# Kernel tuning notes

Measured on AMD Instinct MI355X. Metric: run time of the kernel, lower is better.

Reference implementation:

```python
import jax, jax.numpy as jnp
import numpy as np

B, N, D, H, NB = 64, 2048, 256, 64, 3
TOPK_RATIO = 0.1
LN_EPS = 1e-5
NEG_INF = -1e30


def setup_inputs() -> dict:
    key = jax.random.key(0)
    ks = jax.random.split(key, 16)
    s = 0.02
    return {
        "instances": jax.random.normal(ks[0], (B, N, D), dtype=jnp.float32),
        "mask": jnp.ones((B, N), dtype=jnp.float32),
        # top-k scorer: Linear(D,64) -> ReLU -> Linear(64,1)
        "Ws1": jax.random.normal(ks[1], (D, H), dtype=jnp.float32) * s,
        "bs1": jnp.zeros((H,), dtype=jnp.float32),
        "Ws2": jax.random.normal(ks[2], (H,), dtype=jnp.float32) * s,
        "bs2": jnp.zeros((), dtype=jnp.float32),
        # NB attention branches stacked: Linear(D,64) -> Tanh -> Linear(64,1)
        "Wa1": jax.random.normal(ks[3], (NB, D, H), dtype=jnp.float32) * s,
        "ba1": jnp.zeros((NB, H), dtype=jnp.float32),
        "Wa2": jax.random.normal(ks[4], (NB, H), dtype=jnp.float32) * s,
        "ba2": jnp.zeros((NB,), dtype=jnp.float32),
        # fusion: Linear(5D, 2D) -> LayerNorm -> GELU -> Linear(2D, 2D)
        "Wf1": jax.random.normal(ks[5], ((2 + NB) * D, 2 * D), dtype=jnp.float32) * s,
        "bf1": jnp.zeros((2 * D,), dtype=jnp.float32),
        "ln_g": jnp.ones((2 * D,), dtype=jnp.float32),
        "ln_b": jnp.zeros((2 * D,), dtype=jnp.float32),
        "Wf2": jax.random.normal(ks[6], (2 * D, 2 * D), dtype=jnp.float32) * s,
        "bf2": jnp.zeros((2 * D,), dtype=jnp.float32),
    }


def _forward(instances, mask, Ws1, bs1, Ws2, bs2, Wa1, ba1, Wa2, ba2,
             Wf1, bf1, ln_g, ln_b, Wf2, bf2):
    invalid = mask == 0  # [B, N]

    # ---- mean pooling (masked) ----
    valid_counts = jnp.sum(mask, axis=1, keepdims=True)  # [B,1]
    mean_pooled = jnp.einsum("bnd,bn->bd", instances, mask) / jnp.maximum(valid_counts, 1.0)

    # ---- top-k pooling ----
    h = jax.nn.relu(jnp.einsum("bnd,dh->bnh", instances, Ws1) + bs1)
    tk_scores = jnp.einsum("bnh,h->bn", h, Ws2) + bs2  # [B, N]
    tk_scores = jnp.where(invalid, NEG_INF, tk_scores)
    # torch code computes per-sample k but only uses max_k; with all-ones mask
    # max_k == int(N * ratio) (static) -- replicated faithfully.
    max_k = max(1, int(N * TOPK_RATIO))
    _, topk_idx = jax.lax.top_k(tk_scores, max_k)  # [B, max_k]
    topk_mask = jnp.zeros((B, N), dtype=instances.dtype)
    topk_mask = topk_mask.at[jnp.arange(B)[:, None], topk_idx].set(1.0)
    combined = topk_mask * mask
    denom = jnp.maximum(jnp.sum(combined, axis=1, keepdims=True), 1.0)
    topk_pooled = jnp.einsum("bnd,bn->bd", instances, combined) / denom

    # ---- multi-branch attention (vectorized over branches) ----
    ah = jnp.tanh(jnp.einsum("bnd,kdh->kbnh", instances, Wa1) + ba1[:, None, None, :])
    a_scores = jnp.einsum("kbnh,kh->kbn", ah, Wa2) + ba2[:, None, None]  # [NB,B,N]
    a_scores = jnp.where(invalid[None], NEG_INF, a_scores)
    attn = jax.nn.softmax(a_scores, axis=-1)
    attn = jnp.where(invalid[None], 0.0, attn)  # [NB, B, N]
    branch_pooled = jnp.einsum("kbn,bnd->kbd", attn, instances)  # [NB, B, D]

    # ---- fusion MLP ----
    cat = jnp.concatenate(
        [mean_pooled, topk_pooled, branch_pooled.transpose(1, 0, 2).reshape(B, NB * D)],
        axis=-1,
    )  # [B, (2+NB)*D]
    x = cat @ Wf1 + bf1
    mu = jnp.mean(x, axis=-1, keepdims=True)
    var = jnp.mean(jnp.square(x - mu), axis=-1, keepdims=True)
    x = (x - mu) * jax.lax.rsqrt(var + LN_EPS) * ln_g + ln_b
    x = jax.nn.gelu(x, approximate=False)  # torch nn.GELU default = exact erf
    bag_embedding = x @ Wf2 + bf2  # [B, 2D]

    # ---- attention diagnostics ----
    all_attn = attn.transpose(1, 0, 2)  # [B, NB, N]
    avg_attn = jnp.mean(all_attn, axis=1)  # [B, N]
    entropy = -jnp.sum(avg_attn * jnp.log(avg_attn + 1e-8), axis=-1)
    effective_n = 1.0 / jnp.sum(jnp.square(avg_attn), axis=-1)
    k5 = max(1, int(N * 0.05))
    top5_mass = jnp.sum(jax.lax.top_k(avg_attn, k5)[0], axis=-1)
    return bag_embedding, all_attn, avg_attn, topk_mask, entropy, effective_n, top5_mass


def reference(instances, mask, Ws1, bs1, Ws2, bs2, Wa1, ba1, Wa2, ba2,
              Wf1, bf1, ln_g, ln_b, Wf2, bf2):
    return _forward(instances, mask, Ws1, bs1, Ws2, bs2, Wa1, ba1, Wa2, ba2,
                    Wf1, bf1, ln_g, ln_b, Wf2, bf2)
```

## Files before the change

kernel.cpp:

```cpp
#include <hip/hip_runtime.h>
#include <stdint.h>

constexpr int B_ = 64, N_ = 2048, D_ = 256, H_ = 64;
constexpr int M_ = B_ * N_;
constexpr int TOPK_ = 204, TOP5_ = 102;
constexpr float NEGINF_ = -1e30f;

constexpr int OUT_BAG  = 0;
constexpr int OUT_ATTN = 32768;
constexpr int OUT_AVG  = OUT_ATTN + 393216;
constexpr int OUT_TOPK = OUT_AVG + 131072;
constexpr int OUT_ENT  = OUT_TOPK + 131072;
constexpr int OUT_EFF  = OUT_ENT + 64;
constexpr int OUT_T5   = OUT_EFF + 64;

constexpr int WS_TK    = 0;
constexpr int WS_SC    = 131072;
constexpr int WS_STATS = WS_SC + 393216;
constexpr int WS_PART  = WS_STATS + 128;
constexpr int WS_BFRAG = WS_PART + 655360;
constexpr int WS_X1    = WS_BFRAG + 32768;
constexpr int WS_G     = WS_X1 + 32768;

typedef short  bf16x8 __attribute__((ext_vector_type(8)));
typedef float  f32x4  __attribute__((ext_vector_type(4)));

__device__ __forceinline__ short cvt_bf16(float f) {
    unsigned u = __float_as_uint(f);
    unsigned r = (u + 0x7FFFu + ((u >> 16) & 1u)) >> 16;
    return (short)r;
}
__device__ __forceinline__ unsigned pack_bf16x2(float a, float b) {
    return (unsigned)(unsigned short)cvt_bf16(a) | ((unsigned)(unsigned short)cvt_bf16(b) << 16);
}
__device__ __forceinline__ float tanh_fast(float x) {
    float e = __expf(2.0f * x);
    return 1.0f - 2.0f / (e + 1.0f);
}
__device__ __forceinline__ unsigned flip_f32(float f) {
    unsigned u = __float_as_uint(f);
    return (u & 0x80000000u) ? ~u : (u | 0x80000000u);
}
__device__ __forceinline__ float unflip_f32(unsigned u) {
    unsigned b = (u & 0x80000000u) ? (u & 0x7FFFFFFFu) : ~u;
    return __uint_as_float(b);
}

__device__ __forceinline__ float block_sum256(float v, volatile float* red, int t) {
    #pragma unroll
    for (int off = 32; off; off >>= 1) v += __shfl_xor(v, off, 64);
    __syncthreads();
    if ((t & 63) == 0) red[t >> 6] = v;
    __syncthreads();
    return red[0] + red[1] + red[2] + red[3];
}
__device__ __forceinline__ float block_max256(float v, volatile float* red, int t) {
    #pragma unroll
    for (int off = 32; off; off >>= 1) v = fmaxf(v, __shfl_xor(v, off, 64));
    __syncthreads();
    if ((t & 63) == 0) red[t >> 6] = v;
    __syncthreads();
    return fmaxf(fmaxf(red[0], red[1]), fmaxf(red[2], red[3]));
}

__device__ unsigned radix_kth(const unsigned* key, int n, int k,
                              unsigned* hist, int* sdig, int t, int* rem_out)
{
    unsigned prefix = 0;
    int kk = k;
    #pragma unroll
    for (int pass = 0; pass < 4; ++pass) {
        const int shift = 24 - 8 * pass;
        const unsigned hi_mask = (pass == 0) ? 0u : (0xFFFFFFFFu << (shift + 8));
        hist[t] = 0;
        __syncthreads();
        for (int i = t; i < n; i += 256) {
            unsigned u = key[i];
            if ((u & hi_mask) == (prefix & hi_mask))
                atomicAdd(&hist[(u >> shift) & 0xFFu], 1u);
        }
        __syncthreads();
        for (int s = 1; s < 256; s <<= 1) {
            unsigned v = (t + s < 256) ? hist[t + s] : 0u;
            __syncthreads();
            hist[t] += v;
            __syncthreads();
        }
        if (t == 0) *sdig = 0;
        __syncthreads();
        if ((int)hist[t] >= kk) atomicMax(sdig, t);
        __syncthreads();
        const int dig = *sdig;
        if (dig < 255) kk -= (int)hist[dig + 1];
        prefix |= (unsigned)dig << shift;
        __syncthreads();
    }
    *rem_out = kk;
    return prefix;
}

__global__ __launch_bounds__(256)
void k_prep(const float* __restrict__ Ws1, const float* __restrict__ Wa1,
            short* __restrict__ wsB)
{
    const int id = blockIdx.x * 256 + threadIdx.x;
    if (id >= 16384) return;
    const int lane = id & 63, ct = (id >> 6) & 15, c = id >> 10;
    const int col = ct * 16 + (lane & 15);
    const int kb  = c * 32 + ((lane >> 4) << 3);
    bf16x8 v;
    #pragma unroll
    for (int j = 0; j < 8; ++j) {
        const int k = kb + j;
        float w = (col < 64) ? Ws1[(size_t)k * H_ + col]
                             : Wa1[(((size_t)(col >> 6) - 1) * D_ + k) * H_ + (col & 63)];
        v[j] = cvt_bf16(w);
    }
    *(bf16x8*)(wsB + (size_t)id * 8) = v;
}

__global__ __launch_bounds__(256)
void k_scores(const float* __restrict__ inst, const float* __restrict__ mask,
              const short* __restrict__ wsB,
              const float* __restrict__ bs1, const float* __restrict__ Ws2,
              const float* __restrict__ bs2,
              const float* __restrict__ ba1, const float* __restrict__ Wa2,
              const float* __restrict__ ba2,
              float* __restrict__ ws)
{
    __shared__ unsigned xas[8192];
    const int t = threadIdx.x;
    const int s = t >> 6, l = t & 63;
    const int li = l & 15, qu = l >> 4;
    const int row0 = blockIdx.x * 64;

    {
        const float4* src = (const float4*)(inst + (size_t)row0 * D_);
        #pragma unroll
        for (int i = 0; i < 16; ++i) {
            const int f = i * 256 + t;
            const int row = f >> 6, k4 = f & 63;
            float4 x = src[f];
            const int base = ((k4 >> 3) * 256) + ((row >> 4) * 64) + (((k4 >> 1) & 3) * 16) + (row & 15);
            const int ui = base * 4 + (k4 & 1) * 2;
            xas[ui]     = pack_bf16x2(x.x, x.y);
            xas[ui + 1] = pack_bf16x2(x.z, x.w);
        }
    }
    __syncthreads();

    f32x4 acc[4][4];
    #pragma unroll
    for (int rt = 0; rt < 4; ++rt)
        #pragma unroll
        for (int c4 = 0; c4 < 4; ++c4) acc[rt][c4] = (f32x4){0.f, 0.f, 0.f, 0.f};

    const bf16x8* Bg = (const bf16x8*)wsB;
    bf16x8 bcur[4], bnxt[4];
    #pragma unroll
    for (int c4 = 0; c4 < 4; ++c4) bcur[c4] = Bg[(0 * 16 + s * 4 + c4) * 64 + l];

    #pragma unroll
    for (int c = 0; c < 8; ++c) {
        if (c < 7) {
            #pragma unroll
            for (int c4 = 0; c4 < 4; ++c4) bnxt[c4] = Bg[((c + 1) * 16 + s * 4 + c4) * 64 + l];
        }
        #pragma unroll
        for (int rt = 0; rt < 4; ++rt) {
            bf16x8 a = ((const bf16x8*)xas)[(c * 4 + rt) * 64 + l];
            #pragma unroll
            for (int c4 = 0; c4 < 4; ++c4)
                acc[rt][c4] = __builtin_amdgcn_mfma_f32_16x16x32_bf16(a, bcur[c4], acc[rt][c4], 0, 0, 0);
        }
        #pragma unroll
        for (int c4 = 0; c4 < 4; ++c4) bcur[c4] = bnxt[c4];
    }

    float bias[4], w2v[4];
    #pragma unroll
    for (int c4 = 0; c4 < 4; ++c4) {
        const int h = c4 * 16 + li;
        if (s == 0) { bias[c4] = bs1[h];                w2v[c4] = Ws2[h]; }
        else        { bias[c4] = ba1[(s - 1) * H_ + h]; w2v[c4] = Wa2[(s - 1) * H_ + h]; }
    }
    const float b2 = (s == 0) ? bs2[0] : ba2[s - 1];
    float* dst = (s == 0) ? (ws + WS_TK) : (ws + WS_SC + (size_t)(s - 1) * M_);

    #pragma unroll
    for (int rt = 0; rt < 4; ++rt) {
        #pragma unroll
        for (int i = 0; i < 4; ++i) {
            float p = 0.0f;
            #pragma unroll
            for (int c4 = 0; c4 < 4; ++c4) {
                float v = acc[rt][c4][i] + bias[c4];
                p += (s == 0 ? fmaxf(v, 0.0f) : tanh_fast(v)) * w2v[c4];
            }
            #pragma unroll
            for (int off = 1; off < 16; off <<= 1) p += __shfl_xor(p, off, 64);
            if (li == 0) {
                const int gr = row0 + rt * 16 + qu * 4 + i;
                dst[gr] = (mask[gr] == 0.0f) ? NEGINF_ : (p + b2);
            }
        }
    }
}

__global__ __launch_bounds__(256)
void k_batch(const float* __restrict__ ws_tk, const float* __restrict__ ws_sc,
             const float* __restrict__ mask,
             float* __restrict__ out_topk, float* __restrict__ ws_stats,
             float* __restrict__ out_attn, float* __restrict__ out_avg,
             float* __restrict__ out_ent, float* __restrict__ out_eff,
             float* __restrict__ out_t5)
{
    __shared__ float attn_s[3][N_];
    __shared__ unsigned ukey[N_];
    __shared__ unsigned hist[256];
    __shared__ int sdig, tie_cnt;
    __shared__ float red[4];
    const int b = blockIdx.x, t = threadIdx.x;

    float vsum = 0.0f;
    for (int i = t; i < N_; i += 256) {
        ukey[i] = flip_f32(ws_tk[b * N_ + i]);
        vsum += mask[b * N_ + i];
        out_topk[b * N_ + i] = 0.0f;
    }
    float vs = block_sum256(vsum, red, t);
    if (t == 0) { ws_stats[b] = vs; tie_cnt = 0; }
    __syncthreads();
    int rem;
    unsigned T = radix_kth(ukey, N_, TOPK_, hist, &sdig, t, &rem);
    float csum = 0.0f;
    for (int i = t; i < N_; i += 256) {
        const unsigned u = ukey[i];
        bool take = (u > T);
        if (!take && u == T) take = (atomicAdd(&tie_cnt, 1) < rem);
        if (take) {
            out_topk[b * N_ + i] = 1.0f;
            csum += mask[b * N_ + i];
        }
    }
    float cs = block_sum256(csum, red, t);
    if (t == 0) ws_stats[64 + b] = cs;

    for (int s = 0; s < 3; ++s) {
        const float* src = ws_sc + ((size_t)s * B_ + b) * N_;
        float fv[8];
        float mx = -3.4e38f;
        #pragma unroll
        for (int m = 0; m < 8; ++m) { fv[m] = src[t + 256 * m]; mx = fmaxf(mx, fv[m]); }
        float bm = block_max256(mx, red, t);
        float sm = 0.0f;
        #pragma unroll
        for (int m = 0; m < 8; ++m) { fv[m] = expf(fv[m] - bm); sm += fv[m]; }
        float tot = block_sum256(sm, red, t);
        float inv = 1.0f / tot;
        float* dst = out_attn + ((size_t)b * 3 + s) * N_;
        #pragma unroll
        for (int m = 0; m < 8; ++m) {
            float a = fv[m] * inv;
            attn_s[s][t + 256 * m] = a;
            dst[t + 256 * m] = a;
        }
    }
    __syncthreads();

    float esum = 0.0f, qsum = 0.0f;
    for (int i = t; i < N_; i += 256) {
        float a = (attn_s[0][i] + attn_s[1][i] + attn_s[2][i]) * (1.0f / 3.0f);
        out_avg[b * N_ + i] = a;
        esum -= a * logf(a + 1e-8f);
        qsum += a * a;
        ukey[i] = flip_f32(a);
    }
    float es = block_sum256(esum, red, t);
    float qs = block_sum256(qsum, red, t);
    if (t == 0) { out_ent[b] = es; out_eff[b] = 1.0f / qs; }
    __syncthreads();
    T = radix_kth(ukey, N_, TOP5_, hist, &sdig, t, &rem);
    float tsum = 0.0f;
    for (int i = t; i < N_; i += 256) {
        const unsigned u = ukey[i];
        if (u > T) tsum += unflip_f32(u);
    }
    float ts = block_sum256(tsum, red, t);
    if (t == 0) out_t5[b] = ts + (float)rem * unflip_f32(T);
}

__global__ __launch_bounds__(256)
void k_pool(const float* __restrict__ inst, const float* __restrict__ mask,
            const float* __restrict__ out_topk, const float* __restrict__ out_attn,
            float* __restrict__ ws_part)
{
    __shared__ float wgt[5][256];
    __shared__ float4 partial[4][5][64];
    const int blk = blockIdx.x;
    const int b = blk >> 3, ch = blk & 7;
    const int n0 = ch * 256;
    const int t = threadIdx.x;
    const int w = t >> 6, l = t & 63;
    {
        float mv = mask[b * N_ + n0 + t];
        wgt[0][t] = mv;
        wgt[1][t] = out_topk[b * N_ + n0 + t] * mv;
        const float* ab = out_attn + (size_t)b * 3 * N_ + n0 + t;
        wgt[2][t] = ab[0];
        wgt[3][t] = ab[N_];
        wgt[4][t] = ab[2 * N_];
    }
    __syncthreads();
    float4 a0 = {0,0,0,0}, a1 = {0,0,0,0}, a2 = {0,0,0,0}, a3 = {0,0,0,0}, a4 = {0,0,0,0};
    const float4* xp = (const float4*)(inst + ((size_t)b * N_ + n0 + w * 64) * D_) + l;
    #pragma unroll 4
    for (int nn = 0; nn < 64; ++nn) {
        float4 x = xp[(size_t)nn * 64];
        float w0 = wgt[0][w * 64 + nn], w1 = wgt[1][w * 64 + nn];
        float w2 = wgt[2][w * 64 + nn], w3 = wgt[3][w * 64 + nn];
        float w4 = wgt[4][w * 64 + nn];
        a0.x = fmaf(x.x, w0, a0.x); a0.y = fmaf(x.y, w0, a0.y);
        a0.z = fmaf(x.z, w0, a0.z); a0.w = fmaf(x.w, w0, a0.w);
        a1.x = fmaf(x.x, w1, a1.x); a1.y = fmaf(x.y, w1, a1.y);
        a1.z = fmaf(x.z, w1, a1.z); a1.w = fmaf(x.w, w1, a1.w);
        a2.x = fmaf(x.x, w2, a2.x); a2.y = fmaf(x.y, w2, a2.y);
        a2.z = fmaf(x.z, w2, a2.z); a2.w = fmaf(x.w, w2, a2.w);
        a3.x = fmaf(x.x, w3, a3.x); a3.y = fmaf(x.y, w3, a3.y);
        a3.z = fmaf(x.z, w3, a3.z); a3.w = fmaf(x.w, w3, a3.w);
        a4.x = fmaf(x.x, w4, a4.x); a4.y = fmaf(x.y, w4, a4.y);
        a4.z = fmaf(x.z, w4, a4.z); a4.w = fmaf(x.w, w4, a4.w);
    }
    partial[w][0][l] = a0; partial[w][1][l] = a1; partial[w][2][l] = a2;
    partial[w][3][l] = a3; partial[w][4][l] = a4;
    __syncthreads();
    for (int idx = t; idx < 320; idx += 256) {
        const int j = idx >> 6, l2 = idx & 63;
        float4 s0 = partial[0][j][l2], s1 = partial[1][j][l2];
        float4 s2 = partial[2][j][l2], s3 = partial[3][j][l2];
        float4 sm;
        sm.x = s0.x + s1.x + s2.x + s3.x;
        sm.y = s0.y + s1.y + s2.y + s3.y;
        sm.z = s0.z + s1.z + s2.z + s3.z;
        sm.w = s0.w + s1.w + s2.w + s3.w;
        *(float4*)(ws_part + (size_t)blk * 1280 + j * 256 + l2 * 4) = sm;
    }
}

__global__ __launch_bounds__(256)
void k_fuse1(const float* __restrict__ ws_part, const float* __restrict__ ws_stats,
             const float* __restrict__ Wf1, const float* __restrict__ bf1,
             float* __restrict__ x1)
{
    __shared__ float cl[1280];
    __shared__ float part[256];
    const int blk = blockIdx.x;
    const int b = blk >> 3, c = blk & 7;
    const int t = threadIdx.x;
    const float inv0 = 1.0f / fmaxf(ws_stats[b], 1.0f);
    const float inv1 = 1.0f / fmaxf(ws_stats[64 + b], 1.0f);
    for (int i = t; i < 1280; i += 256) {
        const int j = i >> 8, d = i & 255;
        float s = 0.0f;
        #pragma unroll
        for (int cc = 0; cc < 8; ++cc)
            s += ws_part[((size_t)(b * 8 + cc) * 5 + j) * 256 + d];
        if (j == 0)      s *= inv0;
        else if (j == 1) s *= inv1;
        cl[i] = s;
    }
    __syncthreads();
    const int j = c * 64 + (t & 63);
    const int s = t >> 6;
    float acc = 0.0f;
    const float* wp = Wf1 + (size_t)(s * 320) * 512 + j;
    #pragma unroll 8
    for (int i = 0; i < 320; ++i)
        acc = fmaf(cl[s * 320 + i], wp[(size_t)i * 512], acc);
    part[t] = acc;
    __syncthreads();
    if (t < 64)
        x1[b * 512 + c * 64 + t] =
            part[t] + part[64 + t] + part[128 + t] + part[192 + t] + bf1[c * 64 + t];
}

__global__ __launch_bounds__(256)
void k_fuse2(const float* __restrict__ x1, const float* __restrict__ ln_g,
             const float* __restrict__ ln_b, float* __restrict__ g)
{
    __shared__ float red[4];
    const int b = blockIdx.x, t = threadIdx.x;
    float v0 = x1[b * 512 + t], v1 = x1[b * 512 + 256 + t];
    float mu = block_sum256(v0 + v1, red, t) * (1.0f / 512.0f);
    float d0 = v0 - mu, d1 = v1 - mu;
    float var = block_sum256(d0 * d0 + d1 * d1, red, t) * (1.0f / 512.0f);
    float is = 1.0f / sqrtf(var + 1e-5f);
    float y0 = d0 * is * ln_g[t] + ln_b[t];
    float y1 = d1 * is * ln_g[t + 256] + ln_b[t + 256];
    g[b * 512 + t]       = 0.5f * y0 * (1.0f + erff(y0 * 0.70710678118654752440f));
    g[b * 512 + 256 + t] = 0.5f * y1 * (1.0f + erff(y1 * 0.70710678118654752440f));
}

__global__ __launch_bounds__(256)
void k_fuse3(const float* __restrict__ g, const float* __restrict__ Wf2,
             const float* __restrict__ bf2, float* __restrict__ out_bag)
{
    __shared__ float gl[512];
    __shared__ float part[256];
    const int blk = blockIdx.x;
    const int b = blk >> 3, c = blk & 7;
    const int t = threadIdx.x;
    const int j = c * 64 + (t & 63);
    const int s = t >> 6;
    for (int i = t; i < 512; i += 256) gl[i] = g[b * 512 + i];
    __syncthreads();
    float acc = 0.0f;
    const float* wp = Wf2 + (size_t)(s * 128) * 512 + j;
    #pragma unroll 8
    for (int i = 0; i < 128; ++i)
        acc = fmaf(gl[s * 128 + i], wp[(size_t)i * 512], acc);
    part[t] = acc;
    __syncthreads();
    if (t < 64)
        out_bag[b * 512 + c * 64 + t] =
            part[t] + part[64 + t] + part[128 + t] + part[192 + t] + bf2[c * 64 + t];
}

extern "C" void kernel_launch(void* const* d_in, const int* in_sizes, int n_in,
                              void* d_out, int out_size, void* d_ws, size_t ws_size,
                              hipStream_t stream)
{
    (void)in_sizes; (void)n_in; (void)out_size; (void)ws_size;
    const float* inst = (const float*)d_in[0];
    const float* mask = (const float*)d_in[1];
    const float* Ws1  = (const float*)d_in[2];
    const float* bs1  = (const float*)d_in[3];
    const float* Ws2  = (const float*)d_in[4];
    const float* bs2  = (const float*)d_in[5];
    const float* Wa1  = (const float*)d_in[6];
    const float* ba1  = (const float*)d_in[7];
    const float* Wa2  = (const float*)d_in[8];
    const float* ba2  = (const float*)d_in[9];
    const float* Wf1  = (const float*)d_in[10];
    const float* bf1  = (const float*)d_in[11];
    const float* lng  = (const float*)d_in[12];
    const float* lnb  = (const float*)d_in[13];
    const float* Wf2  = (const float*)d_in[14];
    const float* bf2  = (const float*)d_in[15];

    float* out = (float*)d_out;
    float* ws  = (float*)d_ws;
    short* wsB = (short*)(ws + WS_BFRAG);

    k_prep<<<64, 256, 0, stream>>>(Ws1, Wa1, wsB);
    k_scores<<<M_ / 64, 256, 0, stream>>>(inst, mask, wsB, bs1, Ws2, bs2,
                                          ba1, Wa2, ba2, ws);
    k_batch<<<B_, 256, 0, stream>>>(ws + WS_TK, ws + WS_SC, mask,
                                    out + OUT_TOPK, ws + WS_STATS,
                                    out + OUT_ATTN, out + OUT_AVG,
                                    out + OUT_ENT, out + OUT_EFF, out + OUT_T5);
    k_pool<<<B_ * 8, 256, 0, stream>>>(inst, mask, out + OUT_TOPK, out + OUT_ATTN,
                                       ws + WS_PART);
    k_fuse1<<<B_ * 8, 256, 0, stream>>>(ws + WS_PART, ws + WS_STATS, Wf1, bf1,
                                        ws + WS_X1);
    k_fuse2<<<B_, 256, 0, stream>>>(ws + WS_X1, lng, lnb, ws + WS_G);
    k_fuse3<<<B_ * 8, 256, 0, stream>>>(ws + WS_G, Wf2, bf2, out + OUT_BAG);
}
```

Measured before the change: 347.4 us.

## Keep weight fragments in registers and loop over four row tiles per block

k_scores now loads all 32 B-weight fragments into registers once per block and processes four 64-row tiles per block (512 blocks instead of 2048). This amortises the weight loads across tiles. The instance staging is changed to 32-byte row loads with an XOR-swizzled LDS layout to reduce bank conflicts. Launch bounds request 2 blocks per SM. The large register array (32 bf16x8) plus accumulators adds register pressure and may limit occupancy or cause spills, and the per-tile load is not overlapped with the MFMA work.

```diff
diff --git a/kernel.cpp b/kernel.cpp
--- a/kernel.cpp
+++ b/kernel.cpp
@@ -22,8 +22,9 @@
 constexpr int WS_X1    = WS_BFRAG + 32768;
 constexpr int WS_G     = WS_X1 + 32768;
 
-typedef short  bf16x8 __attribute__((ext_vector_type(8)));
-typedef float  f32x4  __attribute__((ext_vector_type(4)));
+typedef short    bf16x8 __attribute__((ext_vector_type(8)));
+typedef float    f32x4  __attribute__((ext_vector_type(4)));
+typedef unsigned u32x4  __attribute__((ext_vector_type(4)));
 
 __device__ __forceinline__ short cvt_bf16(float f) {
     unsigned u = __float_as_uint(f);
@@ -119,7 +120,7 @@
     *(bf16x8*)(wsB + (size_t)id * 8) = v;
 }
 
-__global__ __launch_bounds__(256)
+__global__ __launch_bounds__(256, 2)
 void k_scores(const float* __restrict__ inst, const float* __restrict__ mask,
               const short* __restrict__ wsB,
               const float* __restrict__ bs1, const float* __restrict__ Ws2,
@@ -132,49 +133,15 @@
     const int t = threadIdx.x;
     const int s = t >> 6, l = t & 63;
     const int li = l & 15, qu = l >> 4;
-    const int row0 = blockIdx.x * 64;
-
+
+    bf16x8 breg[32];
     {
-        const float4* src = (const float4*)(inst + (size_t)row0 * D_);
-        #pragma unroll
-        for (int i = 0; i < 16; ++i) {
-            const int f = i * 256 + t;
-            const int row = f >> 6, k4 = f & 63;
-            float4 x = src[f];
-            const int base = ((k4 >> 3) * 256) + ((row >> 4) * 64) + (((k4 >> 1) & 3) * 16) + (row & 15);
-            const int ui = base * 4 + (k4 & 1) * 2;
-            xas[ui]     = pack_bf16x2(x.x, x.y);
-            xas[ui + 1] = pack_bf16x2(x.z, x.w);
-        }
-    }
-    __syncthreads();
-
-    f32x4 acc[4][4];
-    #pragma unroll
-    for (int rt = 0; rt < 4; ++rt)
-        #pragma unroll
-        for (int c4 = 0; c4 < 4; ++c4) acc[rt][c4] = (f32x4){0.f, 0.f, 0.f, 0.f};
-
-    const bf16x8* Bg = (const bf16x8*)wsB;
-    bf16x8 bcur[4], bnxt[4];
-    #pragma unroll
-    for (int c4 = 0; c4 < 4; ++c4) bcur[c4] = Bg[(0 * 16 + s * 4 + c4) * 64 + l];
-
-    #pragma unroll
-    for (int c = 0; c < 8; ++c) {
-        if (c < 7) {
-            #pragma unroll
-            for (int c4 = 0; c4 < 4; ++c4) bnxt[c4] = Bg[((c + 1) * 16 + s * 4 + c4) * 64 + l];
-        }
-        #pragma unroll
-        for (int rt = 0; rt < 4; ++rt) {
-            bf16x8 a = ((const bf16x8*)xas)[(c * 4 + rt) * 64 + l];
+        const bf16x8* Bg = (const bf16x8*)wsB;
+        #pragma unroll
+        for (int c = 0; c < 8; ++c)
             #pragma unroll
             for (int c4 = 0; c4 < 4; ++c4)
-                acc[rt][c4] = __builtin_amdgcn_mfma_f32_16x16x32_bf16(a, bcur[c4], acc[rt][c4], 0, 0, 0);
-        }
-        #pragma unroll
-        for (int c4 = 0; c4 < 4; ++c4) bcur[c4] = bnxt[c4];
+                breg[c * 4 + c4] = Bg[(c * 16 + s * 4 + c4) * 64 + l];
     }
 
     float bias[4], w2v[4];
@@ -187,21 +154,67 @@
     const float b2 = (s == 0) ? bs2[0] : ba2[s - 1];
     float* dst = (s == 0) ? (ws + WS_TK) : (ws + WS_SC + (size_t)(s - 1) * M_);
 
-    #pragma unroll
-    for (int rt = 0; rt < 4; ++rt) {
-        #pragma unroll
-        for (int i = 0; i < 4; ++i) {
-            float p = 0.0f;
+    const int srow = t >> 5;
+    const int sk0  = 8 * (t & 31);
+    const int sc   = (t & 31) >> 2;
+    const int sq   = t & 3;
+
+    for (int tt = 0; tt < 4; ++tt) {
+        const int row0 = blockIdx.x * 256 + tt * 64;
+        __syncthreads();
+        {
+            const float* xb = inst + (size_t)row0 * D_ + sk0;
             #pragma unroll
-            for (int c4 = 0; c4 < 4; ++c4) {
-                float v = acc[rt][c4][i] + bias[c4];
-                p += (s == 0 ? fmaxf(v, 0.0f) : tanh_fast(v)) * w2v[c4];
+            for (int i = 0; i < 8; ++i) {
+                const float* rp = xb + (size_t)(i * 8 + srow) * D_;
+                float4 x = *(const float4*)rp;
+                float4 y = *(const float4*)(rp + 4);
+                const int lslot = (i & 1) * 8 + srow;
+                const int slot = (sc * 4 + (i >> 1)) * 64 + sq * 16 + (lslot ^ sc);
+                u32x4 v;
+                v[0] = pack_bf16x2(x.x, x.y);
+                v[1] = pack_bf16x2(x.z, x.w);
+                v[2] = pack_bf16x2(y.x, y.y);
+                v[3] = pack_bf16x2(y.z, y.w);
+                *(u32x4*)&xas[slot * 4] = v;
             }
+        }
+        __syncthreads();
+
+        f32x4 acc[4][4];
+        #pragma unroll
+        for (int rt = 0; rt < 4; ++rt)
             #pragma unroll
-            for (int off = 1; off < 16; off <<= 1) p += __shfl_xor(p, off, 64);
-            if (li == 0) {
-                const int gr = row0 + rt * 16 + qu * 4 + i;
-                dst[gr] = (mask[gr] == 0.0f) ? NEGINF_ : (p + b2);
+            for (int c4 = 0; c4 < 4; ++c4) acc[rt][c4] = (f32x4){0.f, 0.f, 0.f, 0.f};
+
+        #pragma unroll
+        for (int c = 0; c < 8; ++c) {
+            #pragma unroll
+            for (int rt = 0; rt < 4; ++rt) {
+                bf16x8 a = ((const bf16x8*)xas)[(c * 4 + rt) * 64 + qu * 16 + (li ^ c)];
+                #pragma unroll
+                for (int c4 = 0; c4 < 4; ++c4)
+                    acc[rt][c4] = __builtin_amdgcn_mfma_f32_16x16x32_bf16(
+                        a, breg[c * 4 + c4], acc[rt][c4], 0, 0, 0);
+            }
+        }
+
+        #pragma unroll
+        for (int rt = 0; rt < 4; ++rt) {
+            #pragma unroll
+            for (int i = 0; i < 4; ++i) {
+                float p = 0.0f;
+                #pragma unroll
+                for (int c4 = 0; c4 < 4; ++c4) {
+                    float v = acc[rt][c4][i] + bias[c4];
+                    p += (s == 0 ? fmaxf(v, 0.0f) : tanh_fast(v)) * w2v[c4];
+                }
+                #pragma unroll
+                for (int off = 1; off < 16; off <<= 1) p += __shfl_xor(p, off, 64);
+                if (li == 0) {
+                    const int gr = row0 + rt * 16 + qu * 4 + i;
+                    dst[gr] = (mask[gr] == 0.0f) ? NEGINF_ : (p + b2);
+                }
             }
         }
     }
@@ -453,8 +466,8 @@
     short* wsB = (short*)(ws + WS_BFRAG);
 
     k_prep<<<64, 256, 0, stream>>>(Ws1, Wa1, wsB);
-    k_scores<<<M_ / 64, 256, 0, stream>>>(inst, mask, wsB, bs1, Ws2, bs2,
-                                          ba1, Wa2, ba2, ws);
+    k_scores<<<512, 256, 0, stream>>>(inst, mask, wsB, bs1, Ws2, bs2,
+                                      ba1, Wa2, ba2, ws);
     k_batch<<<B_, 256, 0, stream>>>(ws + WS_TK, ws + WS_SC, mask,
                                     out + OUT_TOPK, ws + WS_STATS,
                                     out + OUT_ATTN, out + OUT_AVG,
```

After: 353.3 us. Within noise of the previous version (+1.7%).
